# Performance work log

Measured on AMD Instinct MI355X. Metric: run time of the kernel, lower is better.

## Reference

```python
import jax, jax.numpy as jnp
import numpy as np
from jax import lax

B, C_IN, L = 32, 64, 8192
PF = 128


def caudil_conv(x, W, kw, dilation, causal_padding=0):
    """x: (B, C, L); W: (O, kw*C) with layout W[o, c*kw + j] (channel-major).
    Equivalent to the per-timestep sliced-Linear loop: VALID dilated conv."""
    C = x.shape[1]
    if causal_padding:
        x = jnp.pad(x, ((0, 0), (0, 0), (causal_padding, 0)))
    K = W.reshape(-1, C, kw)  # (O, C, kw)
    return lax.conv_general_dilated(
        x, K, window_strides=(1,), padding='VALID', rhs_dilation=(dilation,),
        dimension_numbers=('NCH', 'OIH', 'NCH'))


def setup_inputs() -> dict:
    key = jax.random.key(0)
    ks = jax.random.split(key, 10)
    s = lambda k, shp: (jax.random.normal(k, shp, dtype=jnp.float32) * 0.05)
    return {
        'x': jax.random.normal(ks[0], (B, C_IN, L), dtype=jnp.float32),
        'w7_1': s(ks[1], (6, 3 * C_IN)),
        'w7_3': s(ks[2], (PF, 3 * 6)),
        'w10_1': s(ks[3], (6, 3 * C_IN)),
        'w10_3': s(ks[4], (6, 3 * 6)),
        'w10_5': s(ks[5], (PF, 2 * 6)),
        'w15_1': s(ks[6], (6, 3 * C_IN)),
        'w15_3': s(ks[7], (6, 3 * 6)),
        'w15_5': s(ks[8], (PF, 3 * 6)),
    }


def reference(x, w7_1, w7_3, w10_1, w10_3, w10_5, w15_1, w15_3, w15_5):
    relu = jax.nn.relu
    # branch 7: (3,d1) -> (3,d2)
    m7 = relu(caudil_conv(x, w7_1, 3, 1))
    m7 = relu(caudil_conv(m7, w7_3, 3, 2))
    # branch 10: (3,d1) -> (3,d2) -> (2,d4,pad4)
    m10 = relu(caudil_conv(x, w10_1, 3, 1))
    m10 = relu(caudil_conv(m10, w10_3, 3, 2))
    m10 = relu(caudil_conv(m10, w10_5, 2, 4, causal_padding=4))
    # branch 15: (3,d1) -> (3,d2) -> (3,d4,pad8)
    m15 = relu(caudil_conv(x, w15_1, 3, 1))
    m15 = relu(caudil_conv(m15, w15_3, 3, 2))
    m15 = relu(caudil_conv(m15, w15_5, 3, 4, causal_padding=8))
    return jnp.concatenate([m7, m10, m15], axis=1)  # (B, 3*PF, L-6)
```

## Files before the change

### kernel.cpp

```cpp
#include <hip/hip_runtime.h>

constexpr int Bn   = 32;
constexpr int CIN  = 64;
constexpr int Lx   = 8192;
constexpr int L1   = 8190;
constexpr int LOUT = 8186;
constexpr int NCH  = 384;

constexpr int TB = 256;
constexpr int TT = 256;
constexpr int NTILES = (LOUT + TT - 1) / TT;

constexpr int W7v   = TT + 4;
constexpr int W10Av = TT + 8;
constexpr int W15Av = TT + 12;
constexpr int W10Bv = TT + 4;
constexpr int W15Bv = TT + 8;

__global__ void prep_weights(const float* __restrict__ w7_1,
                             const float* __restrict__ w10_1,
                             const float* __restrict__ w15_1,
                             float* __restrict__ ws) {
    int idx = blockIdx.x * blockDim.x + threadIdx.x;
    if (idx >= 64 * 54) return;
    int ci = idx / 54, r = idx % 54;
    int k = r / 3, j = r % 3;
    const float* src = (k < 6) ? w7_1 : ((k < 12) ? w10_1 : w15_1);
    int kk = (k < 6) ? k : ((k < 12) ? k - 6 : k - 12);
    ws[ci * 64 + r] = src[kk * 192 + ci * 3 + j];
}

__device__ __forceinline__ void store4(float* __restrict__ op, int t,
                                       float a0, float a1, float a2, float a3) {
    a0 = fmaxf(a0, 0.f); a1 = fmaxf(a1, 0.f);
    a2 = fmaxf(a2, 0.f); a3 = fmaxf(a3, 0.f);
    if (t + 3 < LOUT) {
        *(float2*)(op + t)     = make_float2(a0, a1);
        *(float2*)(op + t + 2) = make_float2(a2, a3);
    } else {
        if (t     < LOUT) op[t]     = a0;
        if (t + 1 < LOUT) op[t + 1] = a1;
        if (t + 2 < LOUT) op[t + 2] = a2;
        if (t + 3 < LOUT) op[t + 3] = a3;
    }
}

__global__ __launch_bounds__(TB)
void fused_inception(const float* __restrict__ x,
                     const float* __restrict__ wS1,
                     const float* __restrict__ w7_3,
                     const float* __restrict__ w10_3,
                     const float* __restrict__ w10_5,
                     const float* __restrict__ w15_3,
                     const float* __restrict__ w15_5,
                     float* __restrict__ out) {
    __shared__ float h7  [6 * W7v];
    __shared__ float h10a[6 * W10Av];
    __shared__ float h15a[6 * W15Av];
    __shared__ float h10b[6 * W10Bv];
    __shared__ float h15b[6 * W15Bv];

    const int tid  = threadIdx.x;
    const int tile = blockIdx.x;
    const int b    = blockIdx.y;
    const int t0   = tile * TT;
    const float* xb = x + (size_t)b * CIN * Lx;

    for (int p = tid; p < TT + 12; p += TB) {
        const int s = t0 - 8 + p;
        float acc[18];
        #pragma unroll
        for (int k = 0; k < 18; ++k) acc[k] = 0.f;
        if (s >= 0 && s < L1) {
            const float* xr = xb + s;
            for (int ci = 0; ci < CIN; ++ci) {
                const float x0 = xr[ci * Lx];
                const float x1 = xr[ci * Lx + 1];
                const float x2 = xr[ci * Lx + 2];
                const float* wr = wS1 + ci * 64;
                #pragma unroll
                for (int k = 0; k < 18; ++k) {
                    acc[k] = fmaf(wr[k * 3 + 0], x0, acc[k]);
                    acc[k] = fmaf(wr[k * 3 + 1], x1, acc[k]);
                    acc[k] = fmaf(wr[k * 3 + 2], x2, acc[k]);
                }
            }
            #pragma unroll
            for (int k = 0; k < 18; ++k) acc[k] = fmaxf(acc[k], 0.f);
        }
        if (p >= 8) {
            #pragma unroll
            for (int c = 0; c < 6; ++c) h7[c * W7v + (p - 8)] = acc[c];
        }
        if (p >= 4) {
            #pragma unroll
            for (int c = 0; c < 6; ++c) h10a[c * W10Av + (p - 4)] = acc[6 + c];
        }
        #pragma unroll
        for (int c = 0; c < 6; ++c) h15a[c * W15Av + p] = acc[12 + c];
    }
    __syncthreads();

    for (int p = tid; p < W10Bv; p += TB) {
        const int u = t0 - 4 + p;
        float v[18];
        #pragma unroll
        for (int c = 0; c < 6; ++c)
            #pragma unroll
            for (int j = 0; j < 3; ++j)
                v[c * 3 + j] = h10a[c * W10Av + p + 2 * j];
        #pragma unroll
        for (int k = 0; k < 6; ++k) {
            float a = 0.f;
            #pragma unroll
            for (int r = 0; r < 18; ++r) a = fmaf(w10_3[k * 18 + r], v[r], a);
            h10b[k * W10Bv + p] = (u >= 0) ? fmaxf(a, 0.f) : 0.f;
        }
    }
    for (int p = tid; p < W15Bv; p += TB) {
        const int u = t0 - 8 + p;
        float v[18];
        #pragma unroll
        for (int c = 0; c < 6; ++c)
            #pragma unroll
            for (int j = 0; j < 3; ++j)
                v[c * 3 + j] = h15a[c * W15Av + p + 2 * j];
        #pragma unroll
        for (int k = 0; k < 6; ++k) {
            float a = 0.f;
            #pragma unroll
            for (int r = 0; r < 18; ++r) a = fmaf(w15_3[k * 18 + r], v[r], a);
            h15b[k * W15Bv + p] = (u >= 0) ? fmaxf(a, 0.f) : 0.f;
        }
    }
    __syncthreads();

    const int tq = tid & 63;
    const int wv = tid >> 6;
    const int tt = tq * 4;
    const int tglob = t0 + tt;

    {
        float v[6][8];
        #pragma unroll
        for (int c = 0; c < 6; ++c) {
            float4 A = *(const float4*)&h7[c * W7v + tt];
            float4 Bv = *(const float4*)&h7[c * W7v + tt + 4];
            v[c][0] = A.x; v[c][1] = A.y; v[c][2] = A.z; v[c][3] = A.w;
            v[c][4] = Bv.x; v[c][5] = Bv.y; v[c][6] = Bv.z; v[c][7] = Bv.w;
        }
        for (int oi = 0; oi < 32; ++oi) {
            const int oc = wv * 32 + oi;
            const float* wr = w7_3 + oc * 18;
            float a0 = 0, a1 = 0, a2 = 0, a3 = 0;
            #pragma unroll
            for (int c = 0; c < 6; ++c)
                #pragma unroll
                for (int j = 0; j < 3; ++j) {
                    const float w = wr[c * 3 + j];
                    a0 = fmaf(w, v[c][0 + 2 * j], a0);
                    a1 = fmaf(w, v[c][1 + 2 * j], a1);
                    a2 = fmaf(w, v[c][2 + 2 * j], a2);
                    a3 = fmaf(w, v[c][3 + 2 * j], a3);
                }
            float* op = out + ((size_t)b * NCH + oc) * LOUT;
            store4(op, tglob, a0, a1, a2, a3);
        }
    }
    {
        float v[6][8];
        #pragma unroll
        for (int c = 0; c < 6; ++c) {
            float4 A = *(const float4*)&h10b[c * W10Bv + tt];
            float4 Bv = *(const float4*)&h10b[c * W10Bv + tt + 4];
            v[c][0] = A.x; v[c][1] = A.y; v[c][2] = A.z; v[c][3] = A.w;
            v[c][4] = Bv.x; v[c][5] = Bv.y; v[c][6] = Bv.z; v[c][7] = Bv.w;
        }
        for (int oi = 0; oi < 32; ++oi) {
            const int oc = wv * 32 + oi;
            const float* wr = w10_5 + oc * 12;
            float a0 = 0, a1 = 0, a2 = 0, a3 = 0;
            #pragma unroll
            for (int c = 0; c < 6; ++c) {
                const float w0 = wr[c * 2 + 0];
                const float w1 = wr[c * 2 + 1];
                a0 = fmaf(w0, v[c][0], a0); a0 = fmaf(w1, v[c][4], a0);
                a1 = fmaf(w0, v[c][1], a1); a1 = fmaf(w1, v[c][5], a1);
                a2 = fmaf(w0, v[c][2], a2); a2 = fmaf(w1, v[c][6], a2);
                a3 = fmaf(w0, v[c][3], a3); a3 = fmaf(w1, v[c][7], a3);
            }
            float* op = out + ((size_t)b * NCH + 128 + oc) * LOUT;
            store4(op, tglob, a0, a1, a2, a3);
        }
    }
    {
        float v[6][12];
        #pragma unroll
        for (int c = 0; c < 6; ++c) {
            float4 A = *(const float4*)&h15b[c * W15Bv + tt];
            float4 Bv = *(const float4*)&h15b[c * W15Bv + tt + 4];
            float4 Cv = *(const float4*)&h15b[c * W15Bv + tt + 8];
            v[c][0] = A.x;  v[c][1] = A.y;  v[c][2] = A.z;  v[c][3] = A.w;
            v[c][4] = Bv.x; v[c][5] = Bv.y; v[c][6] = Bv.z; v[c][7] = Bv.w;
            v[c][8] = Cv.x; v[c][9] = Cv.y; v[c][10] = Cv.z; v[c][11] = Cv.w;
        }
        for (int oi = 0; oi < 32; ++oi) {
            const int oc = wv * 32 + oi;
            const float* wr = w15_5 + oc * 18;
            float a0 = 0, a1 = 0, a2 = 0, a3 = 0;
            #pragma unroll
            for (int c = 0; c < 6; ++c)
                #pragma unroll
                for (int j = 0; j < 3; ++j) {
                    const float w = wr[c * 3 + j];
                    a0 = fmaf(w, v[c][0 + 4 * j], a0);
                    a1 = fmaf(w, v[c][1 + 4 * j], a1);
                    a2 = fmaf(w, v[c][2 + 4 * j], a2);
                    a3 = fmaf(w, v[c][3 + 4 * j], a3);
                }
            float* op = out + ((size_t)b * NCH + 256 + oc) * LOUT;
            store4(op, tglob, a0, a1, a2, a3);
        }
    }
}

extern "C" void kernel_launch(void* const* d_in, const int* in_sizes, int n_in,
                              void* d_out, int out_size, void* d_ws, size_t ws_size,
                              hipStream_t stream) {
    const float* x     = (const float*)d_in[0];
    const float* w7_1  = (const float*)d_in[1];
    const float* w7_3  = (const float*)d_in[2];
    const float* w10_1 = (const float*)d_in[3];
    const float* w10_3 = (const float*)d_in[4];
    const float* w10_5 = (const float*)d_in[5];
    const float* w15_1 = (const float*)d_in[6];
    const float* w15_3 = (const float*)d_in[7];
    const float* w15_5 = (const float*)d_in[8];
    float* out = (float*)d_out;
    float* ws  = (float*)d_ws;

    prep_weights<<<dim3(14), dim3(256), 0, stream>>>(w7_1, w10_1, w15_1, ws);
    fused_inception<<<dim3(NTILES, Bn), dim3(TB), 0, stream>>>(
        x, ws, w7_3, w10_3, w10_5, w15_3, w15_5, out);
}
```

Baseline: 527.5 us.

## Split fused kernel into stage12 and stage3 kernels via global intermediate buffer

Replaces the single fused kernel with two kernels. The first computes the first two conv layers per timestep and writes the 18 intermediate channels to a workspace buffer in global memory. The second reads them back and computes the 128-channel output convs, with one block per branch and 8 outputs per thread. The aim is to remove the redundant halo recomputation of the expensive first layer, spread the store-heavy final stage over more blocks, and raise per-thread work for the output stage. In exchange it adds a global round trip for the intermediates and an extra kernel launch.

```diff
diff --git a/kernel.cpp b/kernel.cpp
--- a/kernel.cpp
+++ b/kernel.cpp
@@ -7,15 +7,9 @@
 constexpr int LOUT = 8186;
 constexpr int NCH  = 384;
 
-constexpr int TB = 256;
-constexpr int TT = 256;
-constexpr int NTILES = (LOUT + TT - 1) / TT;
-
-constexpr int W7v   = TT + 4;
-constexpr int W10Av = TT + 8;
-constexpr int W15Av = TT + 12;
-constexpr int W10Bv = TT + 4;
-constexpr int W15Bv = TT + 8;
+constexpr int WS1_OFF = 0;
+constexpr int H_OFF   = 4096;
+constexpr int HSTR    = 8208;
 
 __global__ void prep_weights(const float* __restrict__ w7_1,
                              const float* __restrict__ w10_1,
@@ -27,199 +21,202 @@
     int k = r / 3, j = r % 3;
     const float* src = (k < 6) ? w7_1 : ((k < 12) ? w10_1 : w15_1);
     int kk = (k < 6) ? k : ((k < 12) ? k - 6 : k - 12);
-    ws[ci * 64 + r] = src[kk * 192 + ci * 3 + j];
-}
-
-__device__ __forceinline__ void store4(float* __restrict__ op, int t,
-                                       float a0, float a1, float a2, float a3) {
-    a0 = fmaxf(a0, 0.f); a1 = fmaxf(a1, 0.f);
-    a2 = fmaxf(a2, 0.f); a3 = fmaxf(a3, 0.f);
-    if (t + 3 < LOUT) {
-        *(float2*)(op + t)     = make_float2(a0, a1);
-        *(float2*)(op + t + 2) = make_float2(a2, a3);
-    } else {
-        if (t     < LOUT) op[t]     = a0;
-        if (t + 1 < LOUT) op[t + 1] = a1;
-        if (t + 2 < LOUT) op[t + 2] = a2;
-        if (t + 3 < LOUT) op[t + 3] = a3;
-    }
-}
-
-__global__ __launch_bounds__(TB)
-void fused_inception(const float* __restrict__ x,
-                     const float* __restrict__ wS1,
-                     const float* __restrict__ w7_3,
-                     const float* __restrict__ w10_3,
-                     const float* __restrict__ w10_5,
-                     const float* __restrict__ w15_3,
-                     const float* __restrict__ w15_5,
-                     float* __restrict__ out) {
-    __shared__ float h7  [6 * W7v];
-    __shared__ float h10a[6 * W10Av];
-    __shared__ float h15a[6 * W15Av];
-    __shared__ float h10b[6 * W10Bv];
-    __shared__ float h15b[6 * W15Bv];
-
-    const int tid  = threadIdx.x;
-    const int tile = blockIdx.x;
-    const int b    = blockIdx.y;
-    const int t0   = tile * TT;
+    ws[WS1_OFF + ci * 64 + r] = src[kk * 192 + ci * 3 + j];
+}
+
+constexpr int TTA = 252;
+constexpr int NTA = (L1 + TTA - 1) / TTA;
+
+__global__ __launch_bounds__(256)
+void stage12(const float* __restrict__ x, float* __restrict__ ws,
+             const float* __restrict__ w10_3, const float* __restrict__ w15_3) {
+    __shared__ float a2[12][256];
+    const int tid = threadIdx.x;
+    const int t0  = blockIdx.x * TTA;
+    const int b   = blockIdx.y;
     const float* xb = x + (size_t)b * CIN * Lx;
-
-    for (int p = tid; p < TT + 12; p += TB) {
-        const int s = t0 - 8 + p;
-        float acc[18];
-        #pragma unroll
-        for (int k = 0; k < 18; ++k) acc[k] = 0.f;
-        if (s >= 0 && s < L1) {
-            const float* xr = xb + s;
-            for (int ci = 0; ci < CIN; ++ci) {
-                const float x0 = xr[ci * Lx];
-                const float x1 = xr[ci * Lx + 1];
-                const float x2 = xr[ci * Lx + 2];
-                const float* wr = wS1 + ci * 64;
-                #pragma unroll
-                for (int k = 0; k < 18; ++k) {
-                    acc[k] = fmaf(wr[k * 3 + 0], x0, acc[k]);
-                    acc[k] = fmaf(wr[k * 3 + 1], x1, acc[k]);
-                    acc[k] = fmaf(wr[k * 3 + 2], x2, acc[k]);
-                }
+    float* hb = ws + H_OFF + (size_t)b * 18 * HSTR;
+
+    if (blockIdx.x == 0 && tid < 18 * 8)
+        hb[(tid >> 3) * HSTR + (tid & 7)] = 0.f;
+
+    const int s = t0 + tid;
+    float acc[18];
+    #pragma unroll
+    for (int k = 0; k < 18; ++k) acc[k] = 0.f;
+    if (s < L1) {
+        const float* xr = xb + s;
+        const float* w0 = ws + WS1_OFF;
+        for (int ci = 0; ci < CIN; ++ci) {
+            const float x0 = xr[0];
+            const float x1 = xr[1];
+            const float x2 = xr[2];
+            const float* wr = w0 + ci * 64;
+            #pragma unroll
+            for (int k = 0; k < 18; ++k) {
+                acc[k] = fmaf(wr[k * 3 + 0], x0, acc[k]);
+                acc[k] = fmaf(wr[k * 3 + 1], x1, acc[k]);
+                acc[k] = fmaf(wr[k * 3 + 2], x2, acc[k]);
             }
-            #pragma unroll
-            for (int k = 0; k < 18; ++k) acc[k] = fmaxf(acc[k], 0.f);
-        }
-        if (p >= 8) {
-            #pragma unroll
-            for (int c = 0; c < 6; ++c) h7[c * W7v + (p - 8)] = acc[c];
-        }
-        if (p >= 4) {
-            #pragma unroll
-            for (int c = 0; c < 6; ++c) h10a[c * W10Av + (p - 4)] = acc[6 + c];
-        }
-        #pragma unroll
-        for (int c = 0; c < 6; ++c) h15a[c * W15Av + p] = acc[12 + c];
-    }
+            xr += Lx;
+        }
+        #pragma unroll
+        for (int k = 0; k < 18; ++k) acc[k] = fmaxf(acc[k], 0.f);
+        if (tid < TTA) {
+            #pragma unroll
+            for (int c = 0; c < 6; ++c) hb[c * HSTR + 8 + s] = acc[c];
+        }
+    }
+    #pragma unroll
+    for (int c = 0; c < 12; ++c) a2[c][tid] = acc[6 + c];
     __syncthreads();
 
-    for (int p = tid; p < W10Bv; p += TB) {
-        const int u = t0 - 4 + p;
+    const int u = t0 + tid;
+    if (tid < TTA && u < LOUT) {
         float v[18];
         #pragma unroll
         for (int c = 0; c < 6; ++c)
             #pragma unroll
-            for (int j = 0; j < 3; ++j)
-                v[c * 3 + j] = h10a[c * W10Av + p + 2 * j];
+            for (int j = 0; j < 3; ++j) v[c * 3 + j] = a2[c][tid + 2 * j];
         #pragma unroll
         for (int k = 0; k < 6; ++k) {
             float a = 0.f;
             #pragma unroll
             for (int r = 0; r < 18; ++r) a = fmaf(w10_3[k * 18 + r], v[r], a);
-            h10b[k * W10Bv + p] = (u >= 0) ? fmaxf(a, 0.f) : 0.f;
-        }
-    }
-    for (int p = tid; p < W15Bv; p += TB) {
-        const int u = t0 - 8 + p;
-        float v[18];
-        #pragma unroll
-        for (int c = 0; c < 6; ++c)
-            #pragma unroll
-            for (int j = 0; j < 3; ++j)
-                v[c * 3 + j] = h15a[c * W15Av + p + 2 * j];
+            hb[(6 + k) * HSTR + 8 + u] = fmaxf(a, 0.f);
+        }
+        #pragma unroll
+        for (int c = 0; c < 6; ++c)
+            #pragma unroll
+            for (int j = 0; j < 3; ++j) v[c * 3 + j] = a2[6 + c][tid + 2 * j];
         #pragma unroll
         for (int k = 0; k < 6; ++k) {
             float a = 0.f;
             #pragma unroll
             for (int r = 0; r < 18; ++r) a = fmaf(w15_3[k * 18 + r], v[r], a);
-            h15b[k * W15Bv + p] = (u >= 0) ? fmaxf(a, 0.f) : 0.f;
-        }
+            hb[(12 + k) * HSTR + 8 + u] = fmaxf(a, 0.f);
+        }
+    }
+}
+
+constexpr int TTB = 512;
+constexpr int NTB = 16;
+
+__device__ __forceinline__ void store8(float* __restrict__ op, int t,
+                                       float* __restrict__ a) {
+    #pragma unroll
+    for (int d = 0; d < 8; ++d) a[d] = fmaxf(a[d], 0.f);
+    if (t + 7 < LOUT) {
+        #pragma unroll
+        for (int d = 0; d < 8; d += 2)
+            *(float2*)(op + t + d) = make_float2(a[d], a[d + 1]);
+    } else {
+        #pragma unroll
+        for (int d = 0; d < 8; ++d)
+            if (t + d < LOUT) op[t + d] = a[d];
+    }
+}
+
+__global__ __launch_bounds__(256)
+void stage3(const float* __restrict__ ws,
+            const float* __restrict__ w7_3,
+            const float* __restrict__ w10_5,
+            const float* __restrict__ w15_5,
+            float* __restrict__ out) {
+    __shared__ float hs[6][528];
+    const int tid = threadIdx.x;
+    const int t0  = blockIdx.x * TTB;
+    const int br  = blockIdx.y;
+    const int b   = blockIdx.z;
+    const float* hb = ws + H_OFF + ((size_t)b * 18 + br * 6) * HSTR;
+
+    for (int idx = tid; idx < 6 * 132; idx += 256) {
+        const int c = idx / 132, q = idx - c * 132;
+        *(float4*)&hs[c][q * 4] = *(const float4*)&hb[c * HSTR + t0 + q * 4];
     }
     __syncthreads();
 
-    const int tq = tid & 63;
-    const int wv = tid >> 6;
-    const int tt = tq * 4;
-    const int tglob = t0 + tt;
-
-    {
-        float v[6][8];
-        #pragma unroll
-        for (int c = 0; c < 6; ++c) {
-            float4 A = *(const float4*)&h7[c * W7v + tt];
-            float4 Bv = *(const float4*)&h7[c * W7v + tt + 4];
-            v[c][0] = A.x; v[c][1] = A.y; v[c][2] = A.z; v[c][3] = A.w;
-            v[c][4] = Bv.x; v[c][5] = Bv.y; v[c][6] = Bv.z; v[c][7] = Bv.w;
-        }
+    const int tq  = tid & 63;
+    const int wvU = __builtin_amdgcn_readfirstlane(threadIdx.x >> 6);
+    const int t   = t0 + tq * 8;
+    const int rel = tq * 8;
+
+    if (br == 0) {
+        float v[6][12];
+        #pragma unroll
+        for (int c = 0; c < 6; ++c)
+            #pragma unroll
+            for (int m = 0; m < 12; m += 4)
+                *(float4*)&v[c][m] = *(const float4*)&hs[c][rel + 8 + m];
+        const float* wb = w7_3 + wvU * 32 * 18;
+        float* ob = out + ((size_t)b * NCH + wvU * 32) * LOUT;
+        #pragma unroll 2
         for (int oi = 0; oi < 32; ++oi) {
-            const int oc = wv * 32 + oi;
-            const float* wr = w7_3 + oc * 18;
-            float a0 = 0, a1 = 0, a2 = 0, a3 = 0;
+            const float* wr = wb + oi * 18;
+            float a[8];
+            #pragma unroll
+            for (int d = 0; d < 8; ++d) a[d] = 0.f;
             #pragma unroll
             for (int c = 0; c < 6; ++c)
                 #pragma unroll
                 for (int j = 0; j < 3; ++j) {
                     const float w = wr[c * 3 + j];
-                    a0 = fmaf(w, v[c][0 + 2 * j], a0);
-                    a1 = fmaf(w, v[c][1 + 2 * j], a1);
-                    a2 = fmaf(w, v[c][2 + 2 * j], a2);
-                    a3 = fmaf(w, v[c][3 + 2 * j], a3);
+                    #pragma unroll
+                    for (int d = 0; d < 8; ++d) a[d] = fmaf(w, v[c][d + 2 * j], a[d]);
                 }
-            float* op = out + ((size_t)b * NCH + oc) * LOUT;
-            store4(op, tglob, a0, a1, a2, a3);
-        }
-    }
-    {
-        float v[6][8];
-        #pragma unroll
-        for (int c = 0; c < 6; ++c) {
-            float4 A = *(const float4*)&h10b[c * W10Bv + tt];
-            float4 Bv = *(const float4*)&h10b[c * W10Bv + tt + 4];
-            v[c][0] = A.x; v[c][1] = A.y; v[c][2] = A.z; v[c][3] = A.w;
-            v[c][4] = Bv.x; v[c][5] = Bv.y; v[c][6] = Bv.z; v[c][7] = Bv.w;
-        }
+            store8(ob + (size_t)oi * LOUT, t, a);
+        }
+    } else if (br == 1) {
+        float v[6][12];
+        #pragma unroll
+        for (int c = 0; c < 6; ++c)
+            #pragma unroll
+            for (int m = 0; m < 12; m += 4)
+                *(float4*)&v[c][m] = *(const float4*)&hs[c][rel + 4 + m];
+        const float* wb = w10_5 + wvU * 32 * 12;
+        float* ob = out + ((size_t)b * NCH + 128 + wvU * 32) * LOUT;
+        #pragma unroll 2
         for (int oi = 0; oi < 32; ++oi) {
-            const int oc = wv * 32 + oi;
-            const float* wr = w10_5 + oc * 12;
-            float a0 = 0, a1 = 0, a2 = 0, a3 = 0;
+            const float* wr = wb + oi * 12;
+            float a[8];
+            #pragma unroll
+            for (int d = 0; d < 8; ++d) a[d] = 0.f;
             #pragma unroll
             for (int c = 0; c < 6; ++c) {
                 const float w0 = wr[c * 2 + 0];
                 const float w1 = wr[c * 2 + 1];
-                a0 = fmaf(w0, v[c][0], a0); a0 = fmaf(w1, v[c][4], a0);
-                a1 = fmaf(w0, v[c][1], a1); a1 = fmaf(w1, v[c][5], a1);
-                a2 = fmaf(w0, v[c][2], a2); a2 = fmaf(w1, v[c][6], a2);
-                a3 = fmaf(w0, v[c][3], a3); a3 = fmaf(w1, v[c][7], a3);
+                #pragma unroll
+                for (int d = 0; d < 8; ++d) {
+                    a[d] = fmaf(w0, v[c][d], a[d]);
+                    a[d] = fmaf(w1, v[c][d + 4], a[d]);
+                }
             }
-            float* op = out + ((size_t)b * NCH + 128 + oc) * LOUT;
-            store4(op, tglob, a0, a1, a2, a3);
-        }
-    }
-    {
-        float v[6][12];
-        #pragma unroll
-        for (int c = 0; c < 6; ++c) {
-            float4 A = *(const float4*)&h15b[c * W15Bv + tt];
-            float4 Bv = *(const float4*)&h15b[c * W15Bv + tt + 4];
-            float4 Cv = *(const float4*)&h15b[c * W15Bv + tt + 8];
-            v[c][0] = A.x;  v[c][1] = A.y;  v[c][2] = A.z;  v[c][3] = A.w;
-            v[c][4] = Bv.x; v[c][5] = Bv.y; v[c][6] = Bv.z; v[c][7] = Bv.w;
-            v[c][8] = Cv.x; v[c][9] = Cv.y; v[c][10] = Cv.z; v[c][11] = Cv.w;
-        }
+            store8(ob + (size_t)oi * LOUT, t, a);
+        }
+    } else {
+        float v[6][16];
+        #pragma unroll
+        for (int c = 0; c < 6; ++c)
+            #pragma unroll
+            for (int m = 0; m < 16; m += 4)
+                *(float4*)&v[c][m] = *(const float4*)&hs[c][rel + m];
+        const float* wb = w15_5 + wvU * 32 * 18;
+        float* ob = out + ((size_t)b * NCH + 256 + wvU * 32) * LOUT;
+        #pragma unroll 2
         for (int oi = 0; oi < 32; ++oi) {
-            const int oc = wv * 32 + oi;
-            const float* wr = w15_5 + oc * 18;
-            float a0 = 0, a1 = 0, a2 = 0, a3 = 0;
+            const float* wr = wb + oi * 18;
+            float a[8];
+            #pragma unroll
+            for (int d = 0; d < 8; ++d) a[d] = 0.f;
             #pragma unroll
             for (int c = 0; c < 6; ++c)
                 #pragma unroll
                 for (int j = 0; j < 3; ++j) {
                     const float w = wr[c * 3 + j];
-                    a0 = fmaf(w, v[c][0 + 4 * j], a0);
-                    a1 = fmaf(w, v[c][1 + 4 * j], a1);
-                    a2 = fmaf(w, v[c][2 + 4 * j], a2);
-                    a3 = fmaf(w, v[c][3 + 4 * j], a3);
+                    #pragma unroll
+                    for (int d = 0; d < 8; ++d) a[d] = fmaf(w, v[c][d + 4 * j], a[d]);
                 }
-            float* op = out + ((size_t)b * NCH + 256 + oc) * LOUT;
-            store4(op, tglob, a0, a1, a2, a3);
+            store8(ob + (size_t)oi * LOUT, t, a);
         }
     }
 }
@@ -240,6 +237,6 @@
     float* ws  = (float*)d_ws;
 
     prep_weights<<<dim3(14), dim3(256), 0, stream>>>(w7_1, w10_1, w15_1, ws);
-    fused_inception<<<dim3(NTILES, Bn), dim3(TB), 0, stream>>>(
-        x, ws, w7_3, w10_3, w10_5, w15_3, w15_5, out);
-}
+    stage12<<<dim3(NTA, Bn), dim3(256), 0, stream>>>(x, ws, w10_3, w15_3);
+    stage3<<<dim3(NTB, 3, Bn), dim3(256), 0, stream>>>(ws, w7_3, w10_5, w15_5, out);
+}
```

Result: slower. 643.2 us (+21.9%).
